# Optimization experiments

Measured on AMD Instinct MI355X. Metric: run time of the kernel, lower is better.

The kernel has to match this reference:

```python
import jax, jax.numpy as jnp
import numpy as np

# Model/config dims
N_NODE = 500000   # num_node (item vocab)
D      = 100      # opt.hiddenSize
B      = 512      # batch
S      = 50       # session seq len
NS     = 12       # opt.n_sample neighbors per node
HOP    = 1        # opt.n_iter
STEP   = 1        # opt.step (star-graph propagation steps)
LAST   = 3        # opt.last_len
NADJ   = 12       # adjacent items per last item
SCALE  = 1.0 / np.sqrt(D)


def setup_inputs() -> dict:
    key = jax.random.key(0)
    ks = jax.random.split(key, 16)
    stdv = 1.0 / np.sqrt(D)
    u = lambda k, sh: jax.random.uniform(k, sh, jnp.float32, -stdv, stdv)
    return {
        # forward args
        "inputs":     jax.random.randint(ks[0], (B, S), 0, N_NODE),
        "adj":        jax.random.uniform(ks[1], (B, S, S), jnp.float32),
        "item":       jax.random.randint(ks[2], (B, S), 0, N_NODE),
        "last_items": jax.random.randint(ks[3], (B, LAST), 0, N_NODE),
        "adj_items":  jax.random.randint(ks[4], (B, LAST * NADJ), 0, N_NODE),
        # learned params / buffers
        "embedding": u(ks[5], (N_NODE, D)),
        "s":         u(ks[6], (2, 1)),
        "W_star_a":  u(ks[7], (D, D)),
        "W_star_q":  u(ks[8], (D, D)),
        "W_star_k":  u(ks[9], (D, D)),
        "W_g":       u(ks[10], (2 * D, D)),
        "W_l":       u(ks[11], (D, D)),
        "adj_all":   jax.random.randint(ks[12], (N_NODE, NS), 0, N_NODE),
        "num_w":     jax.random.uniform(ks[13], (N_NODE, NS), jnp.float32),
    }


def _l2norm(x):
    # F.normalize(p=2, dim=-1)
    return x / jnp.maximum(jnp.linalg.norm(x, axis=-1, keepdims=True), 1e-12)


def reference(inputs, adj, item, last_items, adj_items,
              embedding, s, W_star_a, W_star_q, W_star_k, W_g, W_l,
              adj_all, num_w):
    # ----- embedding lookup + padding mask -----
    h = embedding[inputs]                                  # [B,S,D]
    mask = (inputs != 0).astype(h.dtype)                   # [B,S]

    # ----- StarAggregator (local branch): star node + gated propagation -----
    denom = jnp.maximum(mask.sum(-1, keepdims=True), 1.0)
    star = (h * mask[..., None]).sum(1) / denom            # [B,D] masked mean
    hl = h
    for _ in range(STEP):
        h_n = jnp.einsum('bst,btd->bsd', adj, hl @ W_star_a)          # neighbor agg
        gate = jax.nn.sigmoid(
            jnp.einsum('bsd,bd->bs', hl @ W_star_q, star @ W_star_k) * SCALE)
        hl = (1.0 - gate)[..., None] * h_n + gate[..., None] * star[:, None, :]
        beta = jnp.einsum('bsd,bd->bs', hl, star) * SCALE
        beta = jax.nn.softmax(jnp.where(mask > 0, beta, -1e9), axis=1)
        star = jnp.einsum('bs,bsd->bd', beta, hl)
    h_local = hl                                           # [B,S,D]

    # ----- GlobalAggregator (hop=1 neighbor-sampling branch) -----
    flat = inputs.reshape(-1)
    neigh_idx = adj_all[flat].reshape(B, S, NS)            # gathered neighbor ids
    neigh_w = num_w[flat].reshape(B, S, NS)                # co-occurrence weights
    neigh = embedding[neigh_idx]                           # [B,S,NS,D]
    alpha = jax.nn.softmax(neigh_w, axis=-1)
    agg = jnp.einsum('bsn,bsnd->bsd', alpha, neigh)        # weighted neighbor sum
    h_global = jax.nn.relu(jnp.concatenate([h, agg], -1) @ W_g)  # [B,S,D]

    # ----- normalize + (eval-mode dropout = identity) + learned 2-way combine -----
    h_local = _l2norm(h_local)
    h_global = _l2norm(h_global)
    output = jnp.einsum('bsdk,ko->bsdo',
                        jnp.stack([h_local, h_global], axis=-1), s)[..., 0]  # [B,S,D]

    # ----- LastAggregator (last-items attention branch) -----
    item_h = embedding[last_items]                         # [B,L,D]
    adj_h = embedding[adj_items].reshape(B, LAST, -1, D)   # [B,L,NADJ,D]
    q = item_h @ W_l
    att = jax.nn.softmax(jnp.einsum('bld,blnd->bln', q, adj_h) * SCALE, axis=-1)
    aggl = jnp.einsum('bln,blnd->bld', att, adj_h)
    last_hidden = (item_h + aggl).mean(axis=1)             # [B,D]

    return output, last_hidden
```

## Files before the change

### kernel.cpp

```cpp
#include <hip/hip_runtime.h>
#include <hip/hip_bf16.h>

#define B_    512
#define S_    50
#define D_    100
#define NS_   12
#define LAST_ 3
#define NADJ_ 12
#define SCALE_ 0.1f

__global__ __launch_bounds__(256, 2) void fused_kernel(
    const int* __restrict__ inputs,
    const float* __restrict__ adj,
    const float* __restrict__ emb,
    const int* __restrict__ adj_all,
    const float* __restrict__ num_w,
    const float* __restrict__ sW,
    const float* __restrict__ Wa,
    const float* __restrict__ Wq,
    const float* __restrict__ Wk,
    const float* __restrict__ Wg,
    float* __restrict__ out)
{
    __shared__ __align__(16) float hL[S_][D_];
    __shared__ __align__(16) float adjL[S_][S_];
    __shared__ __align__(16) float hwa[S_][D_];
    __shared__ float ssq[S_][25];
    __shared__ float star[D_], kb[D_], kq[D_];
    __shared__ float gate[S_], rinv[S_], rinv2[S_];
    __shared__ int   ids[S_];
    __shared__ int   nid[S_ * NS_];
    __shared__ float alf[S_ * NS_];
    __shared__ float denom;

    const int b = blockIdx.x, t = threadIdx.x;
    const float s0 = sW[0], s1 = sW[1];

    if (t < S_) ids[t] = inputs[b * S_ + t];
    __syncthreads();

    for (int e = t; e < S_ * D_ / 4; e += 256) {
        int s = e / 25, dq = e - s * 25;
        ((float4*)&hL[0][0])[e] = ((const float4*)(emb + ids[s] * D_))[dq];
    }
    for (int e = t; e < S_ * S_ / 4; e += 256) {
        ((float4*)&adjL[0][0])[e] = ((const float4*)(adj + b * S_ * S_))[e];
    }
    __syncthreads();

    if (t == 0) {
        float c = 0.f;
        for (int s = 0; s < S_; ++s) c += (ids[s] != 0) ? 1.f : 0.f;
        denom = fmaxf(c, 1.f);
    }
    __syncthreads();

    if (t < D_) {
        float a = 0.f;
        for (int s = 0; s < S_; ++s) if (ids[s] != 0) a += hL[s][t];
        star[t] = a / denom;
    }
    __syncthreads();

    if (t < D_) {
        float a = 0.f;
        for (int k = 0; k < D_; ++k) a = fmaf(star[k], Wk[k * D_ + t], a);
        kb[t] = a;
    }
    __syncthreads();

    if (t < D_) {
        float a = 0.f;
        const float4* wr = (const float4*)(Wq + t * D_);
#pragma unroll 5
        for (int j = 0; j < 25; ++j) {
            float4 u = wr[j]; int k = j * 4;
            a = fmaf(u.x, kb[k + 0], a);
            a = fmaf(u.y, kb[k + 1], a);
            a = fmaf(u.z, kb[k + 2], a);
            a = fmaf(u.w, kb[k + 3], a);
        }
        kq[t] = a;
    }
    __syncthreads();

    if (t < S_) {
        float a = 0.f;
        for (int k = 0; k < D_; ++k) a = fmaf(hL[t][k], kq[k], a);
        gate[t] = 1.f / (1.f + expf(-a * SCALE_));
    }

    const bool act = (t < 250);
    int sg = 0, dg = 0, sb = 0, d4 = 0;
    if (act) { sg = t / 25; dg = t - sg * 25; sb = sg * 5; d4 = dg * 4; }

    if (act) {
        float acc[5][4] = {};
        for (int k = 0; k < D_; ++k) {
            float4 w = ((const float4*)(Wa + k * D_))[dg];
#pragma unroll
            for (int i = 0; i < 5; ++i) {
                float xv = hL[sb + i][k];
                acc[i][0] = fmaf(xv, w.x, acc[i][0]);
                acc[i][1] = fmaf(xv, w.y, acc[i][1]);
                acc[i][2] = fmaf(xv, w.z, acc[i][2]);
                acc[i][3] = fmaf(xv, w.w, acc[i][3]);
            }
        }
#pragma unroll
        for (int i = 0; i < 5; ++i)
#pragma unroll
            for (int j = 0; j < 4; ++j) hwa[sb + i][d4 + j] = acc[i][j];
    }
    __syncthreads();

    float hl[5][4] = {};
    if (act) {
        for (int k = 0; k < S_; ++k) {
            float4 w = ((const float4*)&hwa[k][0])[dg];
#pragma unroll
            for (int i = 0; i < 5; ++i) {
                float av = adjL[sb + i][k];
                hl[i][0] = fmaf(av, w.x, hl[i][0]);
                hl[i][1] = fmaf(av, w.y, hl[i][1]);
                hl[i][2] = fmaf(av, w.z, hl[i][2]);
                hl[i][3] = fmaf(av, w.w, hl[i][3]);
            }
        }
#pragma unroll
        for (int i = 0; i < 5; ++i) {
            float g = gate[sb + i];
#pragma unroll
            for (int j = 0; j < 4; ++j)
                hl[i][j] = (1.f - g) * hl[i][j] + g * star[d4 + j];
            ssq[sb + i][dg] = hl[i][0]*hl[i][0] + hl[i][1]*hl[i][1]
                            + hl[i][2]*hl[i][2] + hl[i][3]*hl[i][3];
        }
    }
    __syncthreads();

    if (t < S_) {
        float ss = 0.f;
        for (int j = 0; j < 25; ++j) ss += ssq[t][j];
        rinv[t] = s0 / fmaxf(sqrtf(ss), 1e-12f);
    }
    for (int e = t; e < S_ * NS_; e += 256) {
        int r = e / NS_, n = e - r * NS_;
        nid[e] = adj_all[ids[r] * NS_ + n];
        alf[e] = num_w[ids[r] * NS_ + n];
    }
    __syncthreads();

    if (t < S_) {
        float mx = -1e30f;
        for (int n = 0; n < NS_; ++n) mx = fmaxf(mx, alf[t * NS_ + n]);
        float e[NS_]; float sm = 0.f;
        for (int n = 0; n < NS_; ++n) { e[n] = expf(alf[t * NS_ + n] - mx); sm += e[n]; }
        float inv = 1.f / sm;
        for (int n = 0; n < NS_; ++n) alf[t * NS_ + n] = e[n] * inv;
    }
    if (act) {
#pragma unroll
        for (int i = 0; i < 5; ++i) {
            float f = rinv[sb + i];
#pragma unroll
            for (int j = 0; j < 4; ++j) hl[i][j] *= f;
        }
    }
    __syncthreads();

    if (act) {
#pragma unroll
        for (int i = 0; i < 5; ++i) {
            int row = sb + i;
            float a0 = 0.f, a1 = 0.f, a2 = 0.f, a3 = 0.f;
#pragma unroll
            for (int n = 0; n < NS_; ++n) {
                float4 u = ((const float4*)(emb + nid[row * NS_ + n] * D_))[dg];
                float al = alf[row * NS_ + n];
                a0 = fmaf(al, u.x, a0); a1 = fmaf(al, u.y, a1);
                a2 = fmaf(al, u.z, a2); a3 = fmaf(al, u.w, a3);
            }
            hwa[row][d4 + 0] = a0; hwa[row][d4 + 1] = a1;
            hwa[row][d4 + 2] = a2; hwa[row][d4 + 3] = a3;
        }
    }
    __syncthreads();

    float o[5][4] = {};
    if (act) {
        for (int k = 0; k < D_; ++k) {
            float4 w = ((const float4*)(Wg + k * D_))[dg];
#pragma unroll
            for (int i = 0; i < 5; ++i) {
                float xv = hL[sb + i][k];
                o[i][0] = fmaf(xv, w.x, o[i][0]); o[i][1] = fmaf(xv, w.y, o[i][1]);
                o[i][2] = fmaf(xv, w.z, o[i][2]); o[i][3] = fmaf(xv, w.w, o[i][3]);
            }
        }
        for (int k = 0; k < D_; ++k) {
            float4 w = ((const float4*)(Wg + (D_ + k) * D_))[dg];
#pragma unroll
            for (int i = 0; i < 5; ++i) {
                float xv = hwa[sb + i][k];
                o[i][0] = fmaf(xv, w.x, o[i][0]); o[i][1] = fmaf(xv, w.y, o[i][1]);
                o[i][2] = fmaf(xv, w.z, o[i][2]); o[i][3] = fmaf(xv, w.w, o[i][3]);
            }
        }
#pragma unroll
        for (int i = 0; i < 5; ++i) {
#pragma unroll
            for (int j = 0; j < 4; ++j) o[i][j] = fmaxf(o[i][j], 0.f);
            ssq[sb + i][dg] = o[i][0]*o[i][0] + o[i][1]*o[i][1]
                            + o[i][2]*o[i][2] + o[i][3]*o[i][3];
        }
    }
    __syncthreads();

    if (t < S_) {
        float ss = 0.f;
        for (int j = 0; j < 25; ++j) ss += ssq[t][j];
        rinv2[t] = s1 / fmaxf(sqrtf(ss), 1e-12f);
    }
    __syncthreads();

    if (act) {
#pragma unroll
        for (int i = 0; i < 5; ++i) {
            float f = rinv2[sb + i];
            int row = b * S_ + sb + i;
            float4 ov;
            ov.x = hl[i][0] + o[i][0] * f;
            ov.y = hl[i][1] + o[i][1] * f;
            ov.z = hl[i][2] + o[i][2] * f;
            ov.w = hl[i][3] + o[i][3] * f;
            ((float4*)(out + row * D_))[dg] = ov;
        }
    }
}

__global__ __launch_bounds__(128) void last_kernel(
    const int* __restrict__ last_items,
    const int* __restrict__ adj_items,
    const float* __restrict__ emb,
    const float* __restrict__ Wl,
    float* __restrict__ out2)
{
    __shared__ __align__(16) float ih[LAST_][D_];
    __shared__ __align__(16) float ah[LAST_][NADJ_][D_];
    __shared__ float qL[LAST_][D_];
    __shared__ float att[LAST_][NADJ_];
    __shared__ int li[LAST_];
    __shared__ int ai[LAST_ * NADJ_];

    const int b = blockIdx.x, t = threadIdx.x;

    if (t < LAST_) li[t] = last_items[b * LAST_ + t];
    if (t < LAST_ * NADJ_) ai[t] = adj_items[b * LAST_ * NADJ_ + t];
    __syncthreads();

    for (int e = t; e < LAST_ * D_ / 4; e += 128) {
        int l = e / 25, dq = e - l * 25;
        ((float4*)&ih[0][0])[e] = ((const float4*)(emb + li[l] * D_))[dq];
    }
    for (int e = t; e < LAST_ * NADJ_ * D_ / 4; e += 128) {
        int j = e / 25, dq = e - j * 25;
        ((float4*)&ah[0][0][0])[e] = ((const float4*)(emb + ai[j] * D_))[dq];
    }
    __syncthreads();

    for (int e = t; e < LAST_ * D_; e += 128) {
        int l = e / D_, d = e - l * D_;
        float a = 0.f;
        for (int k = 0; k < D_; ++k) a = fmaf(ih[l][k], Wl[k * D_ + d], a);
        qL[l][d] = a;
    }
    __syncthreads();

    if (t < LAST_ * NADJ_) {
        int l = t / NADJ_, n = t - l * NADJ_;
        float a = 0.f;
        for (int d = 0; d < D_; ++d) a = fmaf(qL[l][d], ah[l][n][d], a);
        att[l][n] = a * SCALE_;
    }
    __syncthreads();

    if (t < LAST_) {
        float mx = -1e30f;
        for (int n = 0; n < NADJ_; ++n) mx = fmaxf(mx, att[t][n]);
        float e[NADJ_]; float sm = 0.f;
        for (int n = 0; n < NADJ_; ++n) { e[n] = expf(att[t][n] - mx); sm += e[n]; }
        float inv = 1.f / sm;
        for (int n = 0; n < NADJ_; ++n) att[t][n] = e[n] * inv;
    }
    __syncthreads();

    if (t < D_) {
        float acc = 0.f;
        for (int l = 0; l < LAST_; ++l) {
            float a = ih[l][t];
            for (int n = 0; n < NADJ_; ++n) a = fmaf(att[l][n], ah[l][n][t], a);
            acc += a;
        }
        out2[b * D_ + t] = acc * (1.f / 3.f);
    }
}

extern "C" void kernel_launch(void* const* d_in, const int* in_sizes, int n_in,
                              void* d_out, int out_size, void* d_ws, size_t ws_size,
                              hipStream_t stream) {
    (void)in_sizes; (void)n_in; (void)out_size; (void)d_ws; (void)ws_size;
    const int* inputs     = (const int*)d_in[0];
    const float* adj      = (const float*)d_in[1];
    const int* last_items = (const int*)d_in[3];
    const int* adj_items  = (const int*)d_in[4];
    const float* emb      = (const float*)d_in[5];
    const float* sW       = (const float*)d_in[6];
    const float* Wa       = (const float*)d_in[7];
    const float* Wq       = (const float*)d_in[8];
    const float* Wk       = (const float*)d_in[9];
    const float* Wg       = (const float*)d_in[10];
    const float* Wl       = (const float*)d_in[11];
    const int* adj_all    = (const int*)d_in[12];
    const float* num_w    = (const float*)d_in[13];

    float* out = (float*)d_out;

    fused_kernel<<<B_, 256, 0, stream>>>(inputs, adj, emb, adj_all, num_w,
                                         sW, Wa, Wq, Wk, Wg, out);
    last_kernel<<<B_, 128, 0, stream>>>(last_items, adj_items, emb, Wl,
                                        out + B_ * S_ * D_);
}
```

Before: 368.2 us.

## Merge last-items kernel into main kernel and restructure loads and inner loops

Both kernels now run as one launch of 2*B blocks, where the upper half runs the last-items attention in reused shared memory. The adj tile is no longer staged in shared memory and is read directly from global as float2. Neighbor id and weight gathers and their softmax move earlier so they overlap the star computation. The padding count uses a ballot, the matmul inner loops are unrolled by 4 with float4 shared loads, and launch bounds request 3 blocks per CU. Together these aim to cut launch overhead, shared memory use and barriers, at the cost of uncached adj reads and more register pressure.

```diff
diff --git a/kernel.cpp b/kernel.cpp
--- a/kernel.cpp
+++ b/kernel.cpp
@@ -1,5 +1,4 @@
 #include <hip/hip_runtime.h>
-#include <hip/hip_bf16.h>
 
 #define B_    512
 #define S_    50
@@ -9,7 +8,7 @@
 #define NADJ_ 12
 #define SCALE_ 0.1f
 
-__global__ __launch_bounds__(256, 2) void fused_kernel(
+__global__ __launch_bounds__(256, 3) void fused_all(
     const int* __restrict__ inputs,
     const float* __restrict__ adj,
     const float* __restrict__ emb,
@@ -20,12 +19,14 @@
     const float* __restrict__ Wq,
     const float* __restrict__ Wk,
     const float* __restrict__ Wg,
+    const int* __restrict__ last_items,
+    const int* __restrict__ adj_items,
+    const float* __restrict__ Wl,
     float* __restrict__ out)
 {
     __shared__ __align__(16) float hL[S_][D_];
-    __shared__ __align__(16) float adjL[S_][S_];
     __shared__ __align__(16) float hwa[S_][D_];
-    __shared__ float ssq[S_][25];
+    __shared__ __align__(16) float ssq[S_][25];
     __shared__ float star[D_], kb[D_], kq[D_];
     __shared__ float gate[S_], rinv[S_], rinv2[S_];
     __shared__ int   ids[S_];
@@ -33,32 +34,108 @@
     __shared__ float alf[S_ * NS_];
     __shared__ float denom;
 
-    const int b = blockIdx.x, t = threadIdx.x;
+    const int t = threadIdx.x;
+
+    if (blockIdx.x >= B_) {
+        const int b = blockIdx.x - B_;
+        float* ih  = &hL[0][0];
+        float* ah  = &hL[0][0] + 304;
+        float* qL  = &hwa[0][0];
+        float* att = &ssq[0][0];
+        int*   li  = ids;
+        int*   ai  = nid;
+
+        if (t < LAST_) li[t] = last_items[b * LAST_ + t];
+        if (t < LAST_ * NADJ_) ai[t] = adj_items[b * LAST_ * NADJ_ + t];
+        __syncthreads();
+
+        for (int e = t; e < LAST_ * 25; e += 256) {
+            int l = e / 25, dq = e - l * 25;
+            ((float4*)ih)[e] = ((const float4*)(emb + li[l] * D_))[dq];
+        }
+        for (int e = t; e < LAST_ * NADJ_ * 25; e += 256) {
+            int j = e / 25, dq = e - j * 25;
+            ((float4*)ah)[e] = ((const float4*)(emb + ai[j] * D_))[dq];
+        }
+        __syncthreads();
+
+        for (int e = t; e < LAST_ * D_; e += 256) {
+            int l = e / D_, d = e - l * D_;
+            float a = 0.f;
+            for (int k = 0; k < D_; ++k) a = fmaf(ih[l * D_ + k], Wl[k * D_ + d], a);
+            qL[e] = a;
+        }
+        __syncthreads();
+
+        if (t < LAST_ * NADJ_) {
+            int l = t / NADJ_;
+            const float* ar = ah + t * D_;
+            const float* qr = qL + l * D_;
+            float a = 0.f;
+            for (int d = 0; d < D_; ++d) a = fmaf(qr[d], ar[d], a);
+            att[t] = a * SCALE_;
+        }
+        __syncthreads();
+
+        if (t < LAST_) {
+            float mx = -1e30f;
+            for (int n = 0; n < NADJ_; ++n) mx = fmaxf(mx, att[t * NADJ_ + n]);
+            float ex[NADJ_]; float sm = 0.f;
+            for (int n = 0; n < NADJ_; ++n) { ex[n] = expf(att[t * NADJ_ + n] - mx); sm += ex[n]; }
+            float inv = 1.f / sm;
+            for (int n = 0; n < NADJ_; ++n) att[t * NADJ_ + n] = ex[n] * inv;
+        }
+        __syncthreads();
+
+        if (t < D_) {
+            float acc = 0.f;
+            for (int l = 0; l < LAST_; ++l) {
+                float a = ih[l * D_ + t];
+                for (int n = 0; n < NADJ_; ++n)
+                    a = fmaf(att[l * NADJ_ + n], ah[(l * NADJ_ + n) * D_ + t], a);
+                acc += a;
+            }
+            out[B_ * S_ * D_ + b * D_ + t] = acc * (1.f / 3.f);
+        }
+        return;
+    }
+
+    const int b = blockIdx.x;
     const float s0 = sW[0], s1 = sW[1];
 
     if (t < S_) ids[t] = inputs[b * S_ + t];
     __syncthreads();
 
-    for (int e = t; e < S_ * D_ / 4; e += 256) {
+    if (t < 64) {
+        unsigned long long m = __ballot(t < S_ && ids[t] != 0);
+        if (t == 0) denom = fmaxf((float)__popcll(m), 1.f);
+    }
+    for (int e = t; e < S_ * 25; e += 256) {
         int s = e / 25, dq = e - s * 25;
         ((float4*)&hL[0][0])[e] = ((const float4*)(emb + ids[s] * D_))[dq];
     }
-    for (int e = t; e < S_ * S_ / 4; e += 256) {
-        ((float4*)&adjL[0][0])[e] = ((const float4*)(adj + b * S_ * S_))[e];
-    }
-    __syncthreads();
-
-    if (t == 0) {
-        float c = 0.f;
-        for (int s = 0; s < S_; ++s) c += (ids[s] != 0) ? 1.f : 0.f;
-        denom = fmaxf(c, 1.f);
+    for (int e = t; e < S_ * NS_; e += 256) {
+        int r = e / NS_, n = e - r * NS_;
+        nid[e] = adj_all[ids[r] * NS_ + n];
+        alf[e] = num_w[ids[r] * NS_ + n];
     }
     __syncthreads();
 
     if (t < D_) {
         float a = 0.f;
-        for (int s = 0; s < S_; ++s) if (ids[s] != 0) a += hL[s][t];
+        for (int s = 0; s < S_; ++s) a += (ids[s] != 0) ? hL[s][t] : 0.f;
         star[t] = a / denom;
+    } else if (t >= 128 && t < 128 + S_) {
+        int r = t - 128;
+        float mx = -1e30f;
+#pragma unroll
+        for (int n = 0; n < NS_; ++n) mx = fmaxf(mx, alf[r * NS_ + n]);
+        float ex[NS_]; float sm = 0.f;
+#pragma unroll
+        for (int n = 0; n < NS_; ++n) { ex[n] = expf(alf[r * NS_ + n] - mx); sm += ex[n]; }
+        float inv = 1.f / sm;
+#pragma unroll
+        for (int n = 0; n < NS_; ++n) alf[r * NS_ + n] = ex[n] * inv;
     }
     __syncthreads();
 
@@ -75,10 +152,8 @@
 #pragma unroll 5
         for (int j = 0; j < 25; ++j) {
             float4 u = wr[j]; int k = j * 4;
-            a = fmaf(u.x, kb[k + 0], a);
-            a = fmaf(u.y, kb[k + 1], a);
-            a = fmaf(u.z, kb[k + 2], a);
-            a = fmaf(u.w, kb[k + 3], a);
+            a = fmaf(u.x, kb[k + 0], a); a = fmaf(u.y, kb[k + 1], a);
+            a = fmaf(u.z, kb[k + 2], a); a = fmaf(u.w, kb[k + 3], a);
         }
         kq[t] = a;
     }
@@ -86,7 +161,13 @@
 
     if (t < S_) {
         float a = 0.f;
-        for (int k = 0; k < D_; ++k) a = fmaf(hL[t][k], kq[k], a);
+        const float4* hr = (const float4*)&hL[t][0];
+#pragma unroll 5
+        for (int j = 0; j < 25; ++j) {
+            float4 u = hr[j]; int k = j * 4;
+            a = fmaf(u.x, kq[k + 0], a); a = fmaf(u.y, kq[k + 1], a);
+            a = fmaf(u.z, kq[k + 2], a); a = fmaf(u.w, kq[k + 3], a);
+        }
         gate[t] = 1.f / (1.f + expf(-a * SCALE_));
     }
 
@@ -96,35 +177,42 @@
 
     if (act) {
         float acc[5][4] = {};
-        for (int k = 0; k < D_; ++k) {
-            float4 w = ((const float4*)(Wa + k * D_))[dg];
+        const float4* WaQ = (const float4*)Wa;
+        for (int k = 0; k < D_; k += 4) {
+            float4 w0 = WaQ[(k + 0) * 25 + dg];
+            float4 w1 = WaQ[(k + 1) * 25 + dg];
+            float4 w2 = WaQ[(k + 2) * 25 + dg];
+            float4 w3 = WaQ[(k + 3) * 25 + dg];
 #pragma unroll
             for (int i = 0; i < 5; ++i) {
-                float xv = hL[sb + i][k];
-                acc[i][0] = fmaf(xv, w.x, acc[i][0]);
-                acc[i][1] = fmaf(xv, w.y, acc[i][1]);
-                acc[i][2] = fmaf(xv, w.z, acc[i][2]);
-                acc[i][3] = fmaf(xv, w.w, acc[i][3]);
-            }
-        }
-#pragma unroll
-        for (int i = 0; i < 5; ++i)
-#pragma unroll
-            for (int j = 0; j < 4; ++j) hwa[sb + i][d4 + j] = acc[i][j];
+                float4 x = *(const float4*)&hL[sb + i][k];
+                acc[i][0] = fmaf(x.x,w0.x, fmaf(x.y,w1.x, fmaf(x.z,w2.x, fmaf(x.w,w3.x, acc[i][0]))));
+                acc[i][1] = fmaf(x.x,w0.y, fmaf(x.y,w1.y, fmaf(x.z,w2.y, fmaf(x.w,w3.y, acc[i][1]))));
+                acc[i][2] = fmaf(x.x,w0.z, fmaf(x.y,w1.z, fmaf(x.z,w2.z, fmaf(x.w,w3.z, acc[i][2]))));
+                acc[i][3] = fmaf(x.x,w0.w, fmaf(x.y,w1.w, fmaf(x.z,w2.w, fmaf(x.w,w3.w, acc[i][3]))));
+            }
+        }
+#pragma unroll
+        for (int i = 0; i < 5; ++i) {
+            float4 v; v.x = acc[i][0]; v.y = acc[i][1]; v.z = acc[i][2]; v.w = acc[i][3];
+            *(float4*)&hwa[sb + i][d4] = v;
+        }
     }
     __syncthreads();
 
     float hl[5][4] = {};
     if (act) {
-        for (int k = 0; k < S_; ++k) {
-            float4 w = ((const float4*)&hwa[k][0])[dg];
+        const float* adjp = adj + b * S_ * S_;
+        for (int k = 0; k < S_; k += 2) {
+            float4 w0 = *(const float4*)&hwa[k][d4];
+            float4 w1 = *(const float4*)&hwa[k + 1][d4];
 #pragma unroll
             for (int i = 0; i < 5; ++i) {
-                float av = adjL[sb + i][k];
-                hl[i][0] = fmaf(av, w.x, hl[i][0]);
-                hl[i][1] = fmaf(av, w.y, hl[i][1]);
-                hl[i][2] = fmaf(av, w.z, hl[i][2]);
-                hl[i][3] = fmaf(av, w.w, hl[i][3]);
+                float2 a2 = *(const float2*)(adjp + (sb + i) * S_ + k);
+                hl[i][0] = fmaf(a2.x, w0.x, fmaf(a2.y, w1.x, hl[i][0]));
+                hl[i][1] = fmaf(a2.x, w0.y, fmaf(a2.y, w1.y, hl[i][1]));
+                hl[i][2] = fmaf(a2.x, w0.z, fmaf(a2.y, w1.z, hl[i][2]));
+                hl[i][3] = fmaf(a2.x, w0.w, fmaf(a2.y, w1.w, hl[i][3]));
             }
         }
 #pragma unroll
@@ -141,24 +229,12 @@
 
     if (t < S_) {
         float ss = 0.f;
+#pragma unroll
         for (int j = 0; j < 25; ++j) ss += ssq[t][j];
         rinv[t] = s0 / fmaxf(sqrtf(ss), 1e-12f);
     }
-    for (int e = t; e < S_ * NS_; e += 256) {
-        int r = e / NS_, n = e - r * NS_;
-        nid[e] = adj_all[ids[r] * NS_ + n];
-        alf[e] = num_w[ids[r] * NS_ + n];
-    }
-    __syncthreads();
-
-    if (t < S_) {
-        float mx = -1e30f;
-        for (int n = 0; n < NS_; ++n) mx = fmaxf(mx, alf[t * NS_ + n]);
-        float e[NS_]; float sm = 0.f;
-        for (int n = 0; n < NS_; ++n) { e[n] = expf(alf[t * NS_ + n] - mx); sm += e[n]; }
-        float inv = 1.f / sm;
-        for (int n = 0; n < NS_; ++n) alf[t * NS_ + n] = e[n] * inv;
-    }
+    __syncthreads();
+
     if (act) {
 #pragma unroll
         for (int i = 0; i < 5; ++i) {
@@ -166,10 +242,6 @@
 #pragma unroll
             for (int j = 0; j < 4; ++j) hl[i][j] *= f;
         }
-    }
-    __syncthreads();
-
-    if (act) {
 #pragma unroll
         for (int i = 0; i < 5; ++i) {
             int row = sb + i;
@@ -181,30 +253,41 @@
                 a0 = fmaf(al, u.x, a0); a1 = fmaf(al, u.y, a1);
                 a2 = fmaf(al, u.z, a2); a3 = fmaf(al, u.w, a3);
             }
-            hwa[row][d4 + 0] = a0; hwa[row][d4 + 1] = a1;
-            hwa[row][d4 + 2] = a2; hwa[row][d4 + 3] = a3;
+            float4 v; v.x = a0; v.y = a1; v.z = a2; v.w = a3;
+            *(float4*)&hwa[row][d4] = v;
         }
     }
     __syncthreads();
 
     float o[5][4] = {};
     if (act) {
-        for (int k = 0; k < D_; ++k) {
-            float4 w = ((const float4*)(Wg + k * D_))[dg];
+        const float4* WgQ = (const float4*)Wg;
+        for (int k = 0; k < D_; k += 4) {
+            float4 w0 = WgQ[(k + 0) * 25 + dg];
+            float4 w1 = WgQ[(k + 1) * 25 + dg];
+            float4 w2 = WgQ[(k + 2) * 25 + dg];
+            float4 w3 = WgQ[(k + 3) * 25 + dg];
 #pragma unroll
             for (int i = 0; i < 5; ++i) {
-                float xv = hL[sb + i][k];
-                o[i][0] = fmaf(xv, w.x, o[i][0]); o[i][1] = fmaf(xv, w.y, o[i][1]);
-                o[i][2] = fmaf(xv, w.z, o[i][2]); o[i][3] = fmaf(xv, w.w, o[i][3]);
-            }
-        }
-        for (int k = 0; k < D_; ++k) {
-            float4 w = ((const float4*)(Wg + (D_ + k) * D_))[dg];
+                float4 x = *(const float4*)&hL[sb + i][k];
+                o[i][0] = fmaf(x.x,w0.x, fmaf(x.y,w1.x, fmaf(x.z,w2.x, fmaf(x.w,w3.x, o[i][0]))));
+                o[i][1] = fmaf(x.x,w0.y, fmaf(x.y,w1.y, fmaf(x.z,w2.y, fmaf(x.w,w3.y, o[i][1]))));
+                o[i][2] = fmaf(x.x,w0.z, fmaf(x.y,w1.z, fmaf(x.z,w2.z, fmaf(x.w,w3.z, o[i][2]))));
+                o[i][3] = fmaf(x.x,w0.w, fmaf(x.y,w1.w, fmaf(x.z,w2.w, fmaf(x.w,w3.w, o[i][3]))));
+            }
+        }
+        for (int k = 0; k < D_; k += 4) {
+            float4 w0 = WgQ[(D_ + k + 0) * 25 + dg];
+            float4 w1 = WgQ[(D_ + k + 1) * 25 + dg];
+            float4 w2 = WgQ[(D_ + k + 2) * 25 + dg];
+            float4 w3 = WgQ[(D_ + k + 3) * 25 + dg];
 #pragma unroll
             for (int i = 0; i < 5; ++i) {
-                float xv = hwa[sb + i][k];
-                o[i][0] = fmaf(xv, w.x, o[i][0]); o[i][1] = fmaf(xv, w.y, o[i][1]);
-                o[i][2] = fmaf(xv, w.z, o[i][2]); o[i][3] = fmaf(xv, w.w, o[i][3]);
+                float4 x = *(const float4*)&hwa[sb + i][k];
+                o[i][0] = fmaf(x.x,w0.x, fmaf(x.y,w1.x, fmaf(x.z,w2.x, fmaf(x.w,w3.x, o[i][0]))));
+                o[i][1] = fmaf(x.x,w0.y, fmaf(x.y,w1.y, fmaf(x.z,w2.y, fmaf(x.w,w3.y, o[i][1]))));
+                o[i][2] = fmaf(x.x,w0.z, fmaf(x.y,w1.z, fmaf(x.z,w2.z, fmaf(x.w,w3.z, o[i][2]))));
+                o[i][3] = fmaf(x.x,w0.w, fmaf(x.y,w1.w, fmaf(x.z,w2.w, fmaf(x.w,w3.w, o[i][3]))));
             }
         }
 #pragma unroll
@@ -219,6 +302,7 @@
 
     if (t < S_) {
         float ss = 0.f;
+#pragma unroll
         for (int j = 0; j < 25; ++j) ss += ssq[t][j];
         rinv2[t] = s1 / fmaxf(sqrtf(ss), 1e-12f);
     }
@@ -236,73 +320,6 @@
             ov.w = hl[i][3] + o[i][3] * f;
             ((float4*)(out + row * D_))[dg] = ov;
         }
-    }
-}
-
-__global__ __launch_bounds__(128) void last_kernel(
-    const int* __restrict__ last_items,
-    const int* __restrict__ adj_items,
-    const float* __restrict__ emb,
-    const float* __restrict__ Wl,
-    float* __restrict__ out2)
-{
-    __shared__ __align__(16) float ih[LAST_][D_];
-    __shared__ __align__(16) float ah[LAST_][NADJ_][D_];
-    __shared__ float qL[LAST_][D_];
-    __shared__ float att[LAST_][NADJ_];
-    __shared__ int li[LAST_];
-    __shared__ int ai[LAST_ * NADJ_];
-
-    const int b = blockIdx.x, t = threadIdx.x;
-
-    if (t < LAST_) li[t] = last_items[b * LAST_ + t];
-    if (t < LAST_ * NADJ_) ai[t] = adj_items[b * LAST_ * NADJ_ + t];
-    __syncthreads();
-
-    for (int e = t; e < LAST_ * D_ / 4; e += 128) {
-        int l = e / 25, dq = e - l * 25;
-        ((float4*)&ih[0][0])[e] = ((const float4*)(emb + li[l] * D_))[dq];
-    }
-    for (int e = t; e < LAST_ * NADJ_ * D_ / 4; e += 128) {
-        int j = e / 25, dq = e - j * 25;
-        ((float4*)&ah[0][0][0])[e] = ((const float4*)(emb + ai[j] * D_))[dq];
-    }
-    __syncthreads();
-
-    for (int e = t; e < LAST_ * D_; e += 128) {
-        int l = e / D_, d = e - l * D_;
-        float a = 0.f;
-        for (int k = 0; k < D_; ++k) a = fmaf(ih[l][k], Wl[k * D_ + d], a);
-        qL[l][d] = a;
-    }
-    __syncthreads();
-
-    if (t < LAST_ * NADJ_) {
-        int l = t / NADJ_, n = t - l * NADJ_;
-        float a = 0.f;
-        for (int d = 0; d < D_; ++d) a = fmaf(qL[l][d], ah[l][n][d], a);
-        att[l][n] = a * SCALE_;
-    }
-    __syncthreads();
-
-    if (t < LAST_) {
-        float mx = -1e30f;
-        for (int n = 0; n < NADJ_; ++n) mx = fmaxf(mx, att[t][n]);
-        float e[NADJ_]; float sm = 0.f;
-        for (int n = 0; n < NADJ_; ++n) { e[n] = expf(att[t][n] - mx); sm += e[n]; }
-        float inv = 1.f / sm;
-        for (int n = 0; n < NADJ_; ++n) att[t][n] = e[n] * inv;
-    }
-    __syncthreads();
-
-    if (t < D_) {
-        float acc = 0.f;
-        for (int l = 0; l < LAST_; ++l) {
-            float a = ih[l][t];
-            for (int n = 0; n < NADJ_; ++n) a = fmaf(att[l][n], ah[l][n][t], a);
-            acc += a;
-        }
-        out2[b * D_ + t] = acc * (1.f / 3.f);
     }
 }
 
@@ -326,8 +343,7 @@
 
     float* out = (float*)d_out;
 
-    fused_kernel<<<B_, 256, 0, stream>>>(inputs, adj, emb, adj_all, num_w,
-                                         sW, Wa, Wq, Wk, Wg, out);
-    last_kernel<<<B_, 128, 0, stream>>>(last_items, adj_items, emb, Wl,
-                                        out + B_ * S_ * D_);
+    fused_all<<<2 * B_, 256, 0, stream>>>(inputs, adj, emb, adj_all, num_w,
+                                          sW, Wa, Wq, Wk, Wg,
+                                          last_items, adj_items, Wl, out);
 }
```

Result: faster. 360.8 us (-2.0%).
